# Kernel tuning notes

Hardware: AMD Instinct MI355X
Metric: run time of the kernel (lower is better)

## Reference

```python
import jax, jax.numpy as jnp
import numpy as np
import math

B, L, C, H, CP = 2, 512, 576, 8, 128
C3 = C // 3            # 192
DK = C // H            # 72
DK3 = DK // 3          # 24
DIV = math.sqrt(DK)


def _ln(x, w, b, eps=1e-6):
    m = jnp.mean(x, axis=-1, keepdims=True)
    v = jnp.mean(jnp.square(x - m), axis=-1, keepdims=True)
    return (x - m) * jax.lax.rsqrt(v + eps) * w + b


def setup_inputs() -> dict:
    key = jax.random.key(0)
    ks = jax.random.split(key, 12)
    s = 0.05
    def n(k, shape):
        return jax.random.normal(k, shape, jnp.float32) * s
    return {
        "x": jax.random.normal(ks[0], (B, L, C), jnp.float32),
        "pairX": jax.random.normal(ks[1], (B, L, L, CP), jnp.float32),
        "g": jnp.ones((1,), jnp.float32),
        "ln1_w": jnp.ones((C,), jnp.float32), "ln1_b": jnp.zeros((C,), jnp.float32),
        "ln2_w": jnp.ones((CP,), jnp.float32), "ln2_b": jnp.zeros((CP,), jnp.float32),
        "Wq": n(ks[2], (C3, C3)), "bq": jnp.zeros((C3,), jnp.float32),
        "Wk": n(ks[3], (C3, C3)), "bk": jnp.zeros((C3,), jnp.float32),
        "Wv": n(ks[4], (C3, C3)), "bv": jnp.zeros((C3,), jnp.float32),
        "Wg": n(ks[5], (C3, C3)), "bg": jnp.zeros((C3,), jnp.float32),
        "conv_w": n(ks[6], (3, H, H, 5, 5)), "conv_b": jnp.zeros((3, H), jnp.float32),
        "Wp": n(ks[7], (CP, H)), "bp": jnp.zeros((H,), jnp.float32),
        "Wpr": n(ks[8], (H, CP)), "bpr": jnp.zeros((CP,), jnp.float32),
        "Wo": n(ks[9], (C, C)), "bo": jnp.zeros((C,), jnp.float32),
    }


def reference(x, pairX, g, ln1_w, ln1_b, ln2_w, ln2_b, Wq, bq, Wk, bk, Wv, bv,
              Wg, bg, conv_w, conv_b, Wp, bp, Wpr, bpr, Wo, bo):
    ori_x = x
    xn = _ln(x, ln1_w, ln1_b)                      # [B,L,C]
    pn = _ln(pairX, ln2_w, ln2_b)                  # [B,L,L,CP]

    # split channels into 3 groups: [B,3,L,C3]
    xs = xn.reshape(B, L, 3, C3).transpose(0, 2, 1, 3)

    def proj(W, b):
        y = xs @ W + b                              # [B,3,L,C3]
        return y.reshape(B, 3, L, H, DK3).transpose(0, 1, 3, 2, 4)  # [B,3,H,L,DK3]

    q = proj(Wq, bq)
    k = proj(Wk, bk)
    v = proj(Wv, bv)
    gate = proj(Wg, bg)

    qkMatrix = jnp.einsum('bchld,bchmd->bchlm', q, k)  # [B,3,H,L,L]
    pairBias = (pn @ Wp + bp).transpose(0, 3, 1, 2)[:, None]  # [B,1,H,L,L]
    oriQK = qkMatrix + pairBias                     # [B,3,H,L,L]

    # 3-channel 5x5 conv refinement, summed over the 3 branches -> [B,1,H,L,L]
    dn = ('NCHW', 'OIHW', 'NCHW')
    convQK = sum(
        jax.lax.conv_general_dilated(oriQK[:, i], conv_w[i], (1, 1), 'SAME',
                                     dimension_numbers=dn)
        + conv_b[i][None, :, None, None]
        for i in range(3)
    )[:, None]

    qk = (oriQK + convQK) / DIV                     # [B,3,H,L,L]
    score = jax.nn.softmax(qk, axis=-1)
    h_outs = jnp.einsum('bchlm,bchmd->bchld', score, v) * jax.nn.sigmoid(gate)
    h_outs = h_outs.transpose(0, 3, 1, 2, 4).reshape(B, L, C)

    rawScoreMean = jax.nn.gelu(jnp.mean(qk, axis=1).transpose(0, 2, 3, 1),
                               approximate=False)   # [B,L,L,H]
    out1 = (h_outs @ Wo + bo) + ori_x * g
    out2 = rawScoreMean @ Wpr + bpr                 # [B,L,L,CP]
    return out1, out2
```

## Files before the change

kernel.cpp:

```cpp
#include <hip/hip_runtime.h>
#include <hip/hip_bf16.h>

#define BDIM 2
#define LDIM 512
#define CDIM 576
#define HDIM 8
#define CPD  128
#define DK3  24
#define INV_DIV 0.117851130197757920f

static constexpr size_t OFF_Q    = 0;
static constexpr size_t OFF_K    = 589824;
static constexpr size_t OFF_V    = 1179648;
static constexpr size_t OFF_G    = 1769472;
static constexpr size_t OFF_BIAS = 2359296;
static constexpr size_t OFF_ORI  = OFF_BIAS + 4194304;
static constexpr size_t OFF_QK   = OFF_ORI + 12582912;
static constexpr size_t OFF_H    = OFF_QK + 12582912;
static constexpr size_t OFF_WPH  = OFF_H + 589824;
static constexpr size_t OFF_CS   = OFF_WPH + 1024;
static constexpr size_t OFF_XN   = OFF_QK;

__device__ __forceinline__ float gelu_exact(float v) {
    return 0.5f * v * (1.f + erff(v * 0.70710678118654752f));
}

__global__ __launch_bounds__(256) void k_prep(
    const float* __restrict__ ln2w, const float* __restrict__ ln2b,
    const float* __restrict__ Wp, const float* __restrict__ bp,
    float* __restrict__ wph, float* __restrict__ csum)
{
    __shared__ float wl[1024];
    const int tid = threadIdx.x;
    for (int i = tid; i < 1024; i += 256) {
        int h = i >> 7, d = i & 127;
        float v = ln2w[d] * Wp[d * 8 + h];
        wl[i] = v; wph[i] = v;
    }
    __syncthreads();
    const int h = tid >> 5, c4 = tid & 31;
    float p = wl[h * 128 + c4 * 4] + wl[h * 128 + c4 * 4 + 1]
            + wl[h * 128 + c4 * 4 + 2] + wl[h * 128 + c4 * 4 + 3];
#pragma unroll
    for (int o = 1; o < 32; o <<= 1) p += __shfl_xor(p, o);
    if (c4 == 0) csum[h] = p;
    float q = 0.f;
#pragma unroll
    for (int k = 0; k < 4; ++k) { int d = c4 * 4 + k; q = fmaf(ln2b[d], Wp[d * 8 + h], q); }
#pragma unroll
    for (int o = 1; o < 32; o <<= 1) q += __shfl_xor(q, o);
    if (c4 == 0) csum[8 + h] = q + bp[h];
}

__global__ __launch_bounds__(256) void k_ln(
    const float* __restrict__ x, const float* __restrict__ ln1w, const float* __restrict__ ln1b,
    float* __restrict__ xn)
{
    const int tid = threadIdx.x;
    const int wid = tid >> 6, lane = tid & 63;
    const int row = blockIdx.x * 4 + wid;
    const float* xr = x + (size_t)row * CDIM;
    float vals[9]; float s = 0.f, sq = 0.f;
#pragma unroll
    for (int u = 0; u < 9; ++u) {
        float v = xr[lane + 64 * u];
        vals[u] = v; s += v; sq += v * v;
    }
#pragma unroll
    for (int o = 32; o; o >>= 1) { s += __shfl_xor(s, o); sq += __shfl_xor(sq, o); }
    float m = s * (1.f / 576.f);
    float inv = rsqrtf(sq * (1.f / 576.f) - m * m + 1e-6f);
    float* xo = xn + (size_t)row * CDIM;
#pragma unroll
    for (int u = 0; u < 9; ++u) {
        int idx = lane + 64 * u;
        xo[idx] = (vals[u] - m) * inv * ln1w[idx] + ln1b[idx];
    }
}

__global__ __launch_bounds__(256) void k_proj(
    const float* __restrict__ xn,
    const float* __restrict__ Wq, const float* __restrict__ bq,
    const float* __restrict__ Wk, const float* __restrict__ bk,
    const float* __restrict__ Wv, const float* __restrict__ bv,
    const float* __restrict__ Wg, const float* __restrict__ bg,
    float* __restrict__ qo, float* __restrict__ ko, float* __restrict__ vo, float* __restrict__ go)
{
    __shared__ float As[192 * 64];
    __shared__ float Bs[32 * 192];
    const int tid = threadIdx.x;
    const int bx = blockIdx.x;
    const int mi = bx / 48, rem = bx % 48;
    const int g = rem >> 4, rb = rem & 15;
    const int row0 = rb * 64;

    const float* W  = mi == 0 ? Wq : mi == 1 ? Wk : mi == 2 ? Wv : Wg;
    const float* bb = mi == 0 ? bq : mi == 1 ? bk : mi == 2 ? bv : bg;
    float* op       = mi == 0 ? qo : mi == 1 ? ko : mi == 2 ? vo : go;

    {
        const int r = tid & 63, k4b = tid >> 6;
#pragma unroll
        for (int it = 0; it < 12; ++it) {
            int k4 = k4b + it * 4;
            float4 v = *(const float4*)&xn[(size_t)(row0 + r) * 576 + g * 192 + k4 * 4];
            As[(k4 * 4 + 0) * 64 + r] = v.x;
            As[(k4 * 4 + 1) * 64 + r] = v.y;
            As[(k4 * 4 + 2) * 64 + r] = v.z;
            As[(k4 * 4 + 3) * 64 + r] = v.w;
        }
    }

    const int rg = tid >> 4, cg = tid & 15;
    const int r0 = rg * 4, c0 = cg * 12;
    float acc[4][12] = {};

    for (int kk = 0; kk < 192; kk += 32) {
        __syncthreads();
#pragma unroll
        for (int i = 0; i < 6; ++i) {
            int f = tid + 256 * i;
            int k2 = f / 48, c4 = f % 48;
            *(float4*)&Bs[k2 * 192 + c4 * 4] = *(const float4*)&W[(size_t)(kk + k2) * 192 + c4 * 4];
        }
        __syncthreads();
#pragma unroll
        for (int k2 = 0; k2 < 32; ++k2) {
            const float4 a  = *(const float4*)&As[(kk + k2) * 64 + r0];
            const float4 b0 = *(const float4*)&Bs[k2 * 192 + c0];
            const float4 b1 = *(const float4*)&Bs[k2 * 192 + c0 + 4];
            const float4 b2 = *(const float4*)&Bs[k2 * 192 + c0 + 8];
            const float ar[4] = {a.x, a.y, a.z, a.w};
#pragma unroll
            for (int r = 0; r < 4; ++r) {
                acc[r][0] = fmaf(ar[r], b0.x, acc[r][0]);
                acc[r][1] = fmaf(ar[r], b0.y, acc[r][1]);
                acc[r][2] = fmaf(ar[r], b0.z, acc[r][2]);
                acc[r][3] = fmaf(ar[r], b0.w, acc[r][3]);
                acc[r][4] = fmaf(ar[r], b1.x, acc[r][4]);
                acc[r][5] = fmaf(ar[r], b1.y, acc[r][5]);
                acc[r][6] = fmaf(ar[r], b1.z, acc[r][6]);
                acc[r][7] = fmaf(ar[r], b1.w, acc[r][7]);
                acc[r][8] = fmaf(ar[r], b2.x, acc[r][8]);
                acc[r][9] = fmaf(ar[r], b2.y, acc[r][9]);
                acc[r][10] = fmaf(ar[r], b2.z, acc[r][10]);
                acc[r][11] = fmaf(ar[r], b2.w, acc[r][11]);
            }
        }
    }

    const int h = cg >> 1, d24 = (cg & 1) * 12;
    const float4 bj0 = *(const float4*)&bb[c0];
    const float4 bj1 = *(const float4*)&bb[c0 + 4];
    const float4 bj2 = *(const float4*)&bb[c0 + 8];
#pragma unroll
    for (int r = 0; r < 4; ++r) {
        int row = row0 + r0 + r;
        int b = row >> 9, l = row & 511;
        float* o = op + ((((size_t)b * 3 + g) * HDIM + h) * LDIM + l) * DK3 + d24;
        *(float4*)(o + 0) = make_float4(acc[r][0] + bj0.x, acc[r][1] + bj0.y,
                                        acc[r][2] + bj0.z, acc[r][3] + bj0.w);
        *(float4*)(o + 4) = make_float4(acc[r][4] + bj1.x, acc[r][5] + bj1.y,
                                        acc[r][6] + bj1.z, acc[r][7] + bj1.w);
        *(float4*)(o + 8) = make_float4(acc[r][8] + bj2.x, acc[r][9] + bj2.y,
                                        acc[r][10] + bj2.z, acc[r][11] + bj2.w);
    }
}

__global__ __launch_bounds__(256) void k_pairbias(
    const float* __restrict__ pairX, const float* __restrict__ wph,
    const float* __restrict__ csum, float* __restrict__ bias)
{
    const int row = blockIdx.x * 256 + threadIdx.x;
    const float* rp = pairX + (size_t)row * CPD;

    float acc[8] = {};
    float sum = 0.f, sumsq = 0.f;
    for (int s = 0; s < 8; ++s) {
        float rr[16];
        *(float4*)&rr[0]  = *(const float4*)(rp + s * 16 + 0);
        *(float4*)&rr[4]  = *(const float4*)(rp + s * 16 + 4);
        *(float4*)&rr[8]  = *(const float4*)(rp + s * 16 + 8);
        *(float4*)&rr[12] = *(const float4*)(rp + s * 16 + 12);
#pragma unroll
        for (int k = 0; k < 16; ++k) { sum += rr[k]; sumsq = fmaf(rr[k], rr[k], sumsq); }
        const float* wp_s = wph + s * 16;
#pragma unroll
        for (int h = 0; h < 8; ++h) {
            const float* w = wp_s + h * 128;
#pragma unroll
            for (int k = 0; k < 16; ++k) acc[h] = fmaf(rr[k], w[k], acc[h]);
        }
    }
    const float m = sum * (1.f / 128.f);
    const float inv = rsqrtf(sumsq * (1.f / 128.f) - m * m + 1e-6f);
    const int b = row >> 18;
    const int ij = row & 262143;
    float* bo = bias + ((size_t)b << 21) + ij;
#pragma unroll
    for (int h = 0; h < 8; ++h) {
        float o = inv * (acc[h] - m * csum[h]) + csum[8 + h];
        bo[(size_t)h << 18] = o;
    }
}

__global__ __launch_bounds__(256) void k_qkmat(
    const float* __restrict__ q, const float* __restrict__ k,
    const float* __restrict__ bias, float* __restrict__ oriQK)
{
    __shared__ float Kl[512 * 28];
    __shared__ float Ql[32 * 28];
    const int tid = threadIdx.x;
    const int bch = blockIdx.x >> 4;
    const int itile = blockIdx.x & 15;
    const float* kp = k + (size_t)bch * 512 * 24;
    const float* qp = q + (size_t)bch * 512 * 24 + (size_t)itile * 32 * 24;
    for (int idx = tid; idx < 512 * 24; idx += 256) {
        int j = idx / 24, d = idx - j * 24;
        Kl[j * 28 + d] = kp[idx];
    }
    for (int idx = tid; idx < 32 * 24; idx += 256) {
        int i = idx / 24, d = idx - i * 24;
        Ql[i * 28 + d] = qp[idx];
    }
    __syncthreads();

    const int ti = tid >> 4, tj = tid & 15;
    const int b = bch / 24, h = bch & 7;
    const float* biasp = bias + ((size_t)(b * 8 + h) * 512 + itile * 32) * 512;
    float* outp = oriQK + (size_t)bch * 262144 + (size_t)itile * 32 * 512;

    for (int cc = 0; cc < 4; ++cc) {
        float acc[2][8] = {};
#pragma unroll
        for (int d4 = 0; d4 < 6; ++d4) {
            const float4 q0 = *(const float4*)&Ql[(ti * 2 + 0) * 28 + d4 * 4];
            const float4 q1 = *(const float4*)&Ql[(ti * 2 + 1) * 28 + d4 * 4];
#pragma unroll
            for (int u = 0; u < 8; ++u) {
                const float4 kv = *(const float4*)&Kl[(cc * 128 + u * 16 + tj) * 28 + d4 * 4];
                acc[0][u] = fmaf(q0.x, kv.x, fmaf(q0.y, kv.y, fmaf(q0.z, kv.z, fmaf(q0.w, kv.w, acc[0][u]))));
                acc[1][u] = fmaf(q1.x, kv.x, fmaf(q1.y, kv.y, fmaf(q1.z, kv.z, fmaf(q1.w, kv.w, acc[1][u]))));
            }
        }
#pragma unroll
        for (int r = 0; r < 2; ++r) {
            int i = ti * 2 + r;
#pragma unroll
            for (int u = 0; u < 8; ++u) {
                int j = cc * 128 + u * 16 + tj;
                outp[(size_t)i * 512 + j] = acc[r][u] + biasp[(size_t)i * 512 + j];
            }
        }
    }
}

__global__ __launch_bounds__(256, 2) void k_conv(
    const float* __restrict__ oriQK, const float* __restrict__ convW, const float* __restrict__ convB,
    const float* __restrict__ Wpr, const float* __restrict__ bpr,
    float* __restrict__ qk, float* __restrict__ out2)
{
    __shared__ float tile[8 * 36 * 40];
    __shared__ float gql[8 * 1024];
    const int tid = threadIdx.x;
    const int bx = blockIdx.x;
    const int b = bx >> 8, rem = bx & 255;
    const int i0 = (rem >> 4) * 32, j0 = (rem & 15) * 32;

    const int jg = tid & 7, ii = tid >> 3;
    const int j4 = jg * 4;
    float acc[8][4] = {};
    float cen[3][8][4];

    for (int c = 0; c < 3; ++c) {
        __syncthreads();
        for (int idx = tid; idx < 8 * 1296; idx += 256) {
            int ch = idx / 1296;
            int r = idx - ch * 1296;
            int iw = r / 36, jw = r - iw * 36;
            int gi = i0 - 2 + iw, gj = j0 - 2 + jw;
            float v = 0.f;
            if ((unsigned)gi < 512u && (unsigned)gj < 512u)
                v = oriQK[((size_t)(b * 24 + c * 8 + ch) << 18) + ((size_t)gi << 9) + gj];
            tile[ch * 1440 + iw * 40 + jw] = v;
        }
        __syncthreads();

        const float* wb = convW + c * 1600;
        for (int hi = 0; hi < 8; ++hi) {
            const float* tch = &tile[hi * 1440];
#pragma unroll
            for (int kh = 0; kh < 5; ++kh) {
                const float* trow = &tch[(ii + kh) * 40 + j4];
                float v[8];
                *(float4*)&v[0] = *(const float4*)&trow[0];
                *(float4*)&v[4] = *(const float4*)&trow[4];
#pragma unroll
                for (int kw = 0; kw < 5; ++kw) {
                    const float* wt = wb + hi * 25 + kh * 5 + kw;
                    const float w0 = wt[0],    w1 = wt[200],  w2 = wt[400],  w3 = wt[600];
                    const float w4 = wt[800],  w5 = wt[1000], w6 = wt[1200], w7 = wt[1400];
#pragma unroll
                    for (int j = 0; j < 4; ++j) {
                        float vv = v[kw + j];
                        acc[0][j] = fmaf(w0, vv, acc[0][j]);
                        acc[1][j] = fmaf(w1, vv, acc[1][j]);
                        acc[2][j] = fmaf(w2, vv, acc[2][j]);
                        acc[3][j] = fmaf(w3, vv, acc[3][j]);
                        acc[4][j] = fmaf(w4, vv, acc[4][j]);
                        acc[5][j] = fmaf(w5, vv, acc[5][j]);
                        acc[6][j] = fmaf(w6, vv, acc[6][j]);
                        acc[7][j] = fmaf(w7, vv, acc[7][j]);
                    }
                }
            }
        }
#pragma unroll
        for (int h = 0; h < 8; ++h) {
            const float* tr = &tile[h * 1440 + (ii + 2) * 40 + j4 + 2];
            cen[c][h][0] = tr[0]; cen[c][h][1] = tr[1];
            cen[c][h][2] = tr[2]; cen[c][h][3] = tr[3];
        }
    }

    const int gi = i0 + ii, gj = j0 + j4;
    float* qkb = qk + ((size_t)(b * 24) << 18) + ((size_t)gi << 9) + gj;
#pragma unroll
    for (int h = 0; h < 8; ++h) {
        float cv = convB[h] + convB[8 + h] + convB[16 + h];
        float cj[4];
#pragma unroll
        for (int j = 0; j < 4; ++j) cj[j] = acc[h][j] + cv;
        float mm[4] = {};
#pragma unroll
        for (int c = 0; c < 3; ++c) {
            float4 o = make_float4((cen[c][h][0] + cj[0]) * INV_DIV,
                                   (cen[c][h][1] + cj[1]) * INV_DIV,
                                   (cen[c][h][2] + cj[2]) * INV_DIV,
                                   (cen[c][h][3] + cj[3]) * INV_DIV);
            *(float4*)(qkb + ((size_t)(c * 8 + h) << 18)) = o;
#pragma unroll
            for (int j = 0; j < 4; ++j) mm[j] += cen[c][h][j];
        }
#pragma unroll
        for (int j = 0; j < 4; ++j) {
            float gv = gelu_exact((mm[j] * (1.f / 3.f) + cj[j]) * INV_DIV);
            gql[h * 1024 + ii * 32 + j4 + j] = gv;
        }
    }
    __syncthreads();

    const int pq = tid & 31, pg = tid >> 5;
    float4 wv[8];
#pragma unroll
    for (int h = 0; h < 8; ++h) wv[h] = *(const float4*)&Wpr[h * 128 + pq * 4];
    const float4 bv = *(const float4*)&bpr[pq * 4];

    for (int it = 0; it < 128; ++it) {
        int pos = it * 8 + pg;
        float g8[8];
#pragma unroll
        for (int h = 0; h < 8; ++h) g8[h] = gql[h * 1024 + pos];
        float4 o = bv;
        o.x += g8[0]*wv[0].x + g8[1]*wv[1].x + g8[2]*wv[2].x + g8[3]*wv[3].x
             + g8[4]*wv[4].x + g8[5]*wv[5].x + g8[6]*wv[6].x + g8[7]*wv[7].x;
        o.y += g8[0]*wv[0].y + g8[1]*wv[1].y + g8[2]*wv[2].y + g8[3]*wv[3].y
             + g8[4]*wv[4].y + g8[5]*wv[5].y + g8[6]*wv[6].y + g8[7]*wv[7].y;
        o.z += g8[0]*wv[0].z + g8[1]*wv[1].z + g8[2]*wv[2].z + g8[3]*wv[3].z
             + g8[4]*wv[4].z + g8[5]*wv[5].z + g8[6]*wv[6].z + g8[7]*wv[7].z;
        o.w += g8[0]*wv[0].w + g8[1]*wv[1].w + g8[2]*wv[2].w + g8[3]*wv[3].w
             + g8[4]*wv[4].w + g8[5]*wv[5].w + g8[6]*wv[6].w + g8[7]*wv[7].w;
        int oi = i0 + (pos >> 5), oj = j0 + (pos & 31);
        *(float4*)&out2[(((size_t)(b * 512 + oi) << 9) + oj) * 128 + pq * 4] = o;
    }
}

__global__ __launch_bounds__(256) void k_softmax_pv(
    const float* __restrict__ qk, const float* __restrict__ v, const float* __restrict__ gate,
    float* __restrict__ houts)
{
    __shared__ float Vl[512 * 28];
    const int tid = threadIdx.x;
    const int bch = blockIdx.x >> 4, itile = blockIdx.x & 15;
    const float* vp = v + (size_t)bch * (512 * 24);
    for (int idx = tid; idx < 512 * 24; idx += 256) {
        int j = idx / 24, d = idx - j * 24;
        Vl[j * 28 + d] = vp[idx];
    }
    __syncthreads();

    const int wid = tid >> 6, lane = tid & 63;
    const int b = bch / 24, c = (bch % 24) >> 3, h = bch & 7;
    const int tg = lane >> 3;
    for (int rr = 0; rr < 8; ++rr) {
        const int i = itile * 32 + wid * 8 + rr;
        const float* row = qk + ((size_t)bch * 512 + i) * 512;
        float e[8]; float mx = -1e30f;
#pragma unroll
        for (int u = 0; u < 8; ++u) { e[u] = row[lane + 64 * u]; mx = fmaxf(mx, e[u]); }
#pragma unroll
        for (int o = 32; o; o >>= 1) mx = fmaxf(mx, __shfl_xor(mx, o));
        float s = 0.f;
#pragma unroll
        for (int u = 0; u < 8; ++u) { e[u] = __expf(e[u] - mx); s += e[u]; }
#pragma unroll
        for (int o = 32; o; o >>= 1) s += __shfl_xor(s, o);
        float inv = 1.f / s;

        float4 a4[6] = {};
#pragma unroll
        for (int u = 0; u < 8; ++u) {
            float p = e[u] * inv;
            const float* vr = &Vl[(u * 64 + lane) * 28];
#pragma unroll
            for (int k = 0; k < 6; ++k) {
                float4 vv = *(const float4*)(vr + 4 * k);
                a4[k].x = fmaf(p, vv.x, a4[k].x);
                a4[k].y = fmaf(p, vv.y, a4[k].y);
                a4[k].z = fmaf(p, vv.z, a4[k].z);
                a4[k].w = fmaf(p, vv.w, a4[k].w);
            }
        }
#pragma unroll
        for (int k = 0; k < 6; ++k) {
            a4[k].x += __shfl_xor(a4[k].x, 8);  a4[k].y += __shfl_xor(a4[k].y, 8);
            a4[k].z += __shfl_xor(a4[k].z, 8);  a4[k].w += __shfl_xor(a4[k].w, 8);
            a4[k].x += __shfl_xor(a4[k].x, 16); a4[k].y += __shfl_xor(a4[k].y, 16);
            a4[k].z += __shfl_xor(a4[k].z, 16); a4[k].w += __shfl_xor(a4[k].w, 16);
            a4[k].x += __shfl_xor(a4[k].x, 32); a4[k].y += __shfl_xor(a4[k].y, 32);
            a4[k].z += __shfl_xor(a4[k].z, 32); a4[k].w += __shfl_xor(a4[k].w, 32);
        }
        const float af[24] = {
            a4[0].x, a4[0].y, a4[0].z, a4[0].w, a4[1].x, a4[1].y, a4[1].z, a4[1].w,
            a4[2].x, a4[2].y, a4[2].z, a4[2].w, a4[3].x, a4[3].y, a4[3].z, a4[3].w,
            a4[4].x, a4[4].y, a4[4].z, a4[4].w, a4[5].x, a4[5].y, a4[5].z, a4[5].w };
        float w0 = tg==0?af[0]:tg==1?af[3]:tg==2?af[6]:tg==3?af[9]:tg==4?af[12]:tg==5?af[15]:tg==6?af[18]:af[21];
        float w1 = tg==0?af[1]:tg==1?af[4]:tg==2?af[7]:tg==3?af[10]:tg==4?af[13]:tg==5?af[16]:tg==6?af[19]:af[22];
        float w2 = tg==0?af[2]:tg==1?af[5]:tg==2?af[8]:tg==3?af[11]:tg==4?af[14]:tg==5?af[17]:tg==6?af[20]:af[23];
#pragma unroll
        for (int o = 1; o < 8; o <<= 1) {
            w0 += __shfl_xor(w0, o);
            w1 += __shfl_xor(w1, o);
            w2 += __shfl_xor(w2, o);
        }
        if ((lane & 7) == 0) {
            const int d0 = tg * 3;
            const float* gp = gate + ((size_t)bch * 512 + i) * 24 + d0;
            float* op = houts + ((size_t)(b * 512 + i)) * 576 + c * 192 + h * 24 + d0;
            op[0] = w0 / (1.f + __expf(-gp[0]));
            op[1] = w1 / (1.f + __expf(-gp[1]));
            op[2] = w2 / (1.f + __expf(-gp[2]));
        }
    }
}

__global__ __launch_bounds__(256) void k_out1(
    const float* __restrict__ houts, const float* __restrict__ Wo, const float* __restrict__ bo,
    const float* __restrict__ x, const float* __restrict__ gsc,
    float* __restrict__ out1)
{
    __shared__ float As[32 * 33];
    __shared__ float Bs[32 * 64];
    const int tid = threadIdx.x;
    const int mt = blockIdx.x / 9, nt = blockIdx.x % 9;
    const int m0 = mt * 32, n0 = nt * 64;
    const int tn = tid & 15, tm = tid >> 4;
    float acc[2][4] = {};

    for (int kk = 0; kk < 576; kk += 32) {
        {
            int idx = tid;
#pragma unroll
            for (int i = 0; i < 4; ++i, idx += 256) {
                int k2 = idx & 31, m = idx >> 5;
                As[m * 33 + k2] = houts[(size_t)(m0 + m) * 576 + kk + k2];
            }
        }
        {
            int idx = tid;
#pragma unroll
            for (int i = 0; i < 8; ++i, idx += 256) {
                int n = idx & 63, k2 = idx >> 6;
                Bs[k2 * 64 + n] = Wo[(size_t)(kk + k2) * 576 + n0 + n];
            }
        }
        __syncthreads();
#pragma unroll
        for (int k2 = 0; k2 < 32; ++k2) {
            float a0 = As[(tm * 2 + 0) * 33 + k2];
            float a1 = As[(tm * 2 + 1) * 33 + k2];
            const float4 bv = *(const float4*)&Bs[k2 * 64 + tn * 4];
            acc[0][0] += a0 * bv.x; acc[0][1] += a0 * bv.y; acc[0][2] += a0 * bv.z; acc[0][3] += a0 * bv.w;
            acc[1][0] += a1 * bv.x; acc[1][1] += a1 * bv.y; acc[1][2] += a1 * bv.z; acc[1][3] += a1 * bv.w;
        }
        __syncthreads();
    }

    const float gv = gsc[0];
    const float4 b4 = *(const float4*)&bo[n0 + tn * 4];
#pragma unroll
    for (int r = 0; r < 2; ++r) {
        size_t row = (size_t)m0 + tm * 2 + r;
        size_t off = row * 576 + n0 + tn * 4;
        const float4 x4 = *(const float4*)&x[off];
        float4 o;
        o.x = acc[r][0] + b4.x + x4.x * gv;
        o.y = acc[r][1] + b4.y + x4.y * gv;
        o.z = acc[r][2] + b4.z + x4.z * gv;
        o.w = acc[r][3] + b4.w + x4.w * gv;
        *(float4*)&out1[off] = o;
    }
}

extern "C" void kernel_launch(void* const* d_in, const int* in_sizes, int n_in,
                              void* d_out, int out_size, void* d_ws, size_t ws_size,
                              hipStream_t stream) {
    const float* x     = (const float*)d_in[0];
    const float* pairX = (const float*)d_in[1];
    const float* g     = (const float*)d_in[2];
    const float* ln1w  = (const float*)d_in[3];
    const float* ln1b  = (const float*)d_in[4];
    const float* ln2w  = (const float*)d_in[5];
    const float* ln2b  = (const float*)d_in[6];
    const float* Wq    = (const float*)d_in[7];
    const float* bq    = (const float*)d_in[8];
    const float* Wk    = (const float*)d_in[9];
    const float* bk    = (const float*)d_in[10];
    const float* Wv    = (const float*)d_in[11];
    const float* bv    = (const float*)d_in[12];
    const float* Wg    = (const float*)d_in[13];
    const float* bg    = (const float*)d_in[14];
    const float* convW = (const float*)d_in[15];
    const float* convB = (const float*)d_in[16];
    const float* Wp    = (const float*)d_in[17];
    const float* bp    = (const float*)d_in[18];
    const float* Wpr   = (const float*)d_in[19];
    const float* bpr   = (const float*)d_in[20];
    const float* Wo    = (const float*)d_in[21];
    const float* bo    = (const float*)d_in[22];

    float* ws   = (float*)d_ws;
    float* q    = ws + OFF_Q;
    float* k    = ws + OFF_K;
    float* vv   = ws + OFF_V;
    float* gt   = ws + OFF_G;
    float* bias = ws + OFF_BIAS;
    float* ori  = ws + OFF_ORI;
    float* qkb  = ws + OFF_QK;
    float* xn   = ws + OFF_XN;
    float* hout = ws + OFF_H;
    float* wph  = ws + OFF_WPH;
    float* csum = ws + OFF_CS;

    float* out1 = (float*)d_out;
    float* out2 = out1 + 589824;

    k_prep<<<dim3(1), dim3(256), 0, stream>>>(ln2w, ln2b, Wp, bp, wph, csum);
    k_ln<<<dim3(256), dim3(256), 0, stream>>>(x, ln1w, ln1b, xn);
    k_proj<<<dim3(192), dim3(256), 0, stream>>>(xn, Wq, bq, Wk, bk, Wv, bv, Wg, bg,
                                                q, k, vv, gt);
    k_pairbias<<<dim3(2048), dim3(256), 0, stream>>>(pairX, wph, csum, bias);
    k_qkmat<<<dim3(768), dim3(256), 0, stream>>>(q, k, bias, ori);
    k_conv<<<dim3(512), dim3(256), 0, stream>>>(ori, convW, convB, Wpr, bpr, qkb, out2);
    k_softmax_pv<<<dim3(768), dim3(256), 0, stream>>>(qkb, vv, gt, hout);
    k_out1<<<dim3(288), dim3(256), 0, stream>>>(hout, Wo, bo, x, g, out1);
}
```

Measured before the change: 460.8 us.

## Split conv input-channel reduction across two thread halves in k_conv

Doubles k_conv's block size to 512 threads. Each half of the block convolves half of the input heads, and the partial sums are reduced through shared memory. The epilogue then runs on the first half only, and all 512 threads share the Wpr projection loop. This raises parallelism within each of the 512 blocks to hide latency, at the cost of an extra shared-memory reduction, more synchronisation, and idle threads during the epilogue.

Result: no change. 470.0 us (+2.0%).

```diff
diff --git a/kernel.cpp b/kernel.cpp
--- a/kernel.cpp
+++ b/kernel.cpp
@@ -255,26 +255,27 @@
     }
 }
 
-__global__ __launch_bounds__(256, 2) void k_conv(
+__global__ __launch_bounds__(512, 4) void k_conv(
     const float* __restrict__ oriQK, const float* __restrict__ convW, const float* __restrict__ convB,
     const float* __restrict__ Wpr, const float* __restrict__ bpr,
     float* __restrict__ qk, float* __restrict__ out2)
 {
     __shared__ float tile[8 * 36 * 40];
-    __shared__ float gql[8 * 1024];
+    __shared__ float scratch[8192];
     const int tid = threadIdx.x;
     const int bx = blockIdx.x;
     const int b = bx >> 8, rem = bx & 255;
     const int i0 = (rem >> 4) * 32, j0 = (rem & 15) * 32;
 
-    const int jg = tid & 7, ii = tid >> 3;
+    const int jg = tid & 7, ii = (tid >> 3) & 31;
+    const int rep = tid >> 8;
     const int j4 = jg * 4;
     float acc[8][4] = {};
     float cen[3][8][4];
 
     for (int c = 0; c < 3; ++c) {
         __syncthreads();
-        for (int idx = tid; idx < 8 * 1296; idx += 256) {
+        for (int idx = tid; idx < 8 * 1296; idx += 512) {
             int ch = idx / 1296;
             int r = idx - ch * 1296;
             int iw = r / 36, jw = r - iw * 36;
@@ -287,7 +288,7 @@
         __syncthreads();
 
         const float* wb = convW + c * 1600;
-        for (int hi = 0; hi < 8; ++hi) {
+        for (int hi = rep; hi < 8; hi += 2) {
             const float* tch = &tile[hi * 1440];
 #pragma unroll
             for (int kh = 0; kh < 5; ++kh) {
@@ -315,37 +316,61 @@
                 }
             }
         }
+        if (rep == 0) {
+#pragma unroll
+            for (int h = 0; h < 8; ++h) {
+                const float* tr = &tile[h * 1440 + (ii + 2) * 40 + j4 + 2];
+                cen[c][h][0] = tr[0]; cen[c][h][1] = tr[1];
+                cen[c][h][2] = tr[2]; cen[c][h][3] = tr[3];
+            }
+        }
+    }
+
+    if (rep == 1) {
+        const int s = tid - 256;
+#pragma unroll
+        for (int h = 0; h < 8; ++h)
+#pragma unroll
+            for (int j = 0; j < 4; ++j)
+                scratch[(h * 4 + j) * 256 + s] = acc[h][j];
+    }
+    __syncthreads();
+    if (rep == 0) {
+#pragma unroll
+        for (int h = 0; h < 8; ++h)
+#pragma unroll
+            for (int j = 0; j < 4; ++j)
+                acc[h][j] += scratch[(h * 4 + j) * 256 + tid];
+    }
+    __syncthreads();
+
+    float* gql = scratch;
+    if (rep == 0) {
+        const int gi = i0 + ii, gj = j0 + j4;
+        float* qkb = qk + ((size_t)(b * 24) << 18) + ((size_t)gi << 9) + gj;
 #pragma unroll
         for (int h = 0; h < 8; ++h) {
-            const float* tr = &tile[h * 1440 + (ii + 2) * 40 + j4 + 2];
-            cen[c][h][0] = tr[0]; cen[c][h][1] = tr[1];
-            cen[c][h][2] = tr[2]; cen[c][h][3] = tr[3];
-        }
-    }
-
-    const int gi = i0 + ii, gj = j0 + j4;
-    float* qkb = qk + ((size_t)(b * 24) << 18) + ((size_t)gi << 9) + gj;
-#pragma unroll
-    for (int h = 0; h < 8; ++h) {
-        float cv = convB[h] + convB[8 + h] + convB[16 + h];
-        float cj[4];
-#pragma unroll
-        for (int j = 0; j < 4; ++j) cj[j] = acc[h][j] + cv;
-        float mm[4] = {};
-#pragma unroll
-        for (int c = 0; c < 3; ++c) {
-            float4 o = make_float4((cen[c][h][0] + cj[0]) * INV_DIV,
-                                   (cen[c][h][1] + cj[1]) * INV_DIV,
-                                   (cen[c][h][2] + cj[2]) * INV_DIV,
-                                   (cen[c][h][3] + cj[3]) * INV_DIV);
-            *(float4*)(qkb + ((size_t)(c * 8 + h) << 18)) = o;
-#pragma unroll
-            for (int j = 0; j < 4; ++j) mm[j] += cen[c][h][j];
-        }
-#pragma unroll
-        for (int j = 0; j < 4; ++j) {
-            float gv = gelu_exact((mm[j] * (1.f / 3.f) + cj[j]) * INV_DIV);
-            gql[h * 1024 + ii * 32 + j4 + j] = gv;
+            float cv = convB[h] + convB[8 + h] + convB[16 + h];
+            float cj[4];
+#pragma unroll
+            for (int j = 0; j < 4; ++j) cj[j] = acc[h][j] + cv;
+            float mm[4] = {};
+#pragma unroll
+            for (int c = 0; c < 3; ++c) {
+                float4 o = make_float4((cen[c][h][0] + cj[0]) * INV_DIV,
+                                       (cen[c][h][1] + cj[1]) * INV_DIV,
+                                       (cen[c][h][2] + cj[2]) * INV_DIV,
+                                       (cen[c][h][3] + cj[3]) * INV_DIV);
+                *(float4*)(qkb + ((size_t)(c * 8 + h) << 18)) = o;
+#pragma unroll
+                for (int j = 0; j < 4; ++j) mm[j] += cen[c][h][j];
+            }
+            float4 gv4;
+            gv4.x = gelu_exact((mm[0] * (1.f / 3.f) + cj[0]) * INV_DIV);
+            gv4.y = gelu_exact((mm[1] * (1.f / 3.f) + cj[1]) * INV_DIV);
+            gv4.z = gelu_exact((mm[2] * (1.f / 3.f) + cj[2]) * INV_DIV);
+            gv4.w = gelu_exact((mm[3] * (1.f / 3.f) + cj[3]) * INV_DIV);
+            *(float4*)&gql[h * 1024 + ii * 32 + j4] = gv4;
         }
     }
     __syncthreads();
@@ -356,8 +381,8 @@
     for (int h = 0; h < 8; ++h) wv[h] = *(const float4*)&Wpr[h * 128 + pq * 4];
     const float4 bv = *(const float4*)&bpr[pq * 4];
 
-    for (int it = 0; it < 128; ++it) {
-        int pos = it * 8 + pg;
+    for (int it = 0; it < 64; ++it) {
+        int pos = it * 16 + pg;
         float g8[8];
 #pragma unroll
         for (int h = 0; h < 8; ++h) g8[h] = gql[h * 1024 + pos];
@@ -561,7 +586,7 @@
                                                 q, k, vv, gt);
     k_pairbias<<<dim3(2048), dim3(256), 0, stream>>>(pairX, wph, csum, bias);
     k_qkmat<<<dim3(768), dim3(256), 0, stream>>>(q, k, bias, ori);
-    k_conv<<<dim3(512), dim3(256), 0, stream>>>(ori, convW, convB, Wpr, bpr, qkb, out2);
+    k_conv<<<dim3(512), dim3(512), 0, stream>>>(ori, convW, convB, Wpr, bpr, qkb, out2);
     k_softmax_pv<<<dim3(768), dim3(256), 0, stream>>>(qkb, vv, gt, hout);
     k_out1<<<dim3(288), dim3(256), 0, stream>>>(hout, Wo, bo, x, g, out1);
 }
```

## Cut k_conv registers and LDS, stage transposed conv weights, use nontemporal stores

Applied to the files above, without the earlier changes.

The conv kernel now copies the conv weights into shared memory in an [hi][tap][h] layout, so each tap's eight output-channel weights come in as two float4 LDS reads instead of eight scalar global loads. The per-c center values are no longer kept in registers; they are re-read from global oriQK in the epilogue. The gelu staging buffer reuses the tile array, which frees LDS and, with launch bounds raised to 3 blocks per CU, is meant to increase occupancy. The out1/out2 writes become nontemporal stores, at the cost of extra global reads of oriQK and possible register spills under the tighter bound.

Measured after the change: 430.8 us. 6.5% less time.

```diff
diff --git a/kernel.cpp b/kernel.cpp
--- a/kernel.cpp
+++ b/kernel.cpp
@@ -23,6 +23,12 @@
 
 __device__ __forceinline__ float gelu_exact(float v) {
     return 0.5f * v * (1.f + erff(v * 0.70710678118654752f));
+}
+
+typedef float __attribute__((ext_vector_type(4))) f32x4;
+__device__ __forceinline__ void nt_store4(float* p, float a, float b, float c, float d) {
+    f32x4 t = {a, b, c, d};
+    __builtin_nontemporal_store(t, (f32x4*)p);
 }
 
 __global__ __launch_bounds__(256) void k_prep(
@@ -255,13 +261,13 @@
     }
 }
 
-__global__ __launch_bounds__(256, 2) void k_conv(
+__global__ __launch_bounds__(256, 3) void k_conv(
     const float* __restrict__ oriQK, const float* __restrict__ convW, const float* __restrict__ convB,
     const float* __restrict__ Wpr, const float* __restrict__ bpr,
     float* __restrict__ qk, float* __restrict__ out2)
 {
     __shared__ float tile[8 * 36 * 40];
-    __shared__ float gql[8 * 1024];
+    __shared__ float wT[1600];
     const int tid = threadIdx.x;
     const int bx = blockIdx.x;
     const int b = bx >> 8, rem = bx & 255;
@@ -270,10 +276,14 @@
     const int jg = tid & 7, ii = tid >> 3;
     const int j4 = jg * 4;
     float acc[8][4] = {};
-    float cen[3][8][4];
 
     for (int c = 0; c < 3; ++c) {
         __syncthreads();
+        for (int i = tid; i < 1600; i += 256) {
+            int h = i & 7, rest = i >> 3;
+            int tap = rest % 25, hi = rest / 25;
+            wT[hi * 200 + tap * 8 + h] = convW[c * 1600 + h * 200 + hi * 25 + tap];
+        }
         for (int idx = tid; idx < 8 * 1296; idx += 256) {
             int ch = idx / 1296;
             int r = idx - ch * 1296;
@@ -286,9 +296,9 @@
         }
         __syncthreads();
 
-        const float* wb = convW + c * 1600;
         for (int hi = 0; hi < 8; ++hi) {
             const float* tch = &tile[hi * 1440];
+            const float* wch = &wT[hi * 200];
 #pragma unroll
             for (int kh = 0; kh < 5; ++kh) {
                 const float* trow = &tch[(ii + kh) * 40 + j4];
@@ -297,57 +307,66 @@
                 *(float4*)&v[4] = *(const float4*)&trow[4];
 #pragma unroll
                 for (int kw = 0; kw < 5; ++kw) {
-                    const float* wt = wb + hi * 25 + kh * 5 + kw;
-                    const float w0 = wt[0],    w1 = wt[200],  w2 = wt[400],  w3 = wt[600];
-                    const float w4 = wt[800],  w5 = wt[1000], w6 = wt[1200], w7 = wt[1400];
+                    const float4 wA = *(const float4*)&wch[(kh * 5 + kw) * 8];
+                    const float4 wB = *(const float4*)&wch[(kh * 5 + kw) * 8 + 4];
 #pragma unroll
                     for (int j = 0; j < 4; ++j) {
                         float vv = v[kw + j];
-                        acc[0][j] = fmaf(w0, vv, acc[0][j]);
-                        acc[1][j] = fmaf(w1, vv, acc[1][j]);
-                        acc[2][j] = fmaf(w2, vv, acc[2][j]);
-                        acc[3][j] = fmaf(w3, vv, acc[3][j]);
-                        acc[4][j] = fmaf(w4, vv, acc[4][j]);
-                        acc[5][j] = fmaf(w5, vv, acc[5][j]);
-                        acc[6][j] = fmaf(w6, vv, acc[6][j]);
-                        acc[7][j] = fmaf(w7, vv, acc[7][j]);
+                        acc[0][j] = fmaf(wA.x, vv, acc[0][j]);
+                        acc[1][j] = fmaf(wA.y, vv, acc[1][j]);
+                        acc[2][j] = fmaf(wA.z, vv, acc[2][j]);
+                        acc[3][j] = fmaf(wA.w, vv, acc[3][j]);
+                        acc[4][j] = fmaf(wB.x, vv, acc[4][j]);
+                        acc[5][j] = fmaf(wB.y, vv, acc[5][j]);
+                        acc[6][j] = fmaf(wB.z, vv, acc[6][j]);
+                        acc[7][j] = fmaf(wB.w, vv, acc[7][j]);
                     }
                 }
             }
         }
-#pragma unroll
-        for (int h = 0; h < 8; ++h) {
-            const float* tr = &tile[h * 1440 + (ii + 2) * 40 + j4 + 2];
-            cen[c][h][0] = tr[0]; cen[c][h][1] = tr[1];
-            cen[c][h][2] = tr[2]; cen[c][h][3] = tr[3];
-        }
     }
 
     const int gi = i0 + ii, gj = j0 + j4;
+    const float* orib = oriQK + ((size_t)(b * 24) << 18) + ((size_t)gi << 9) + gj;
     float* qkb = qk + ((size_t)(b * 24) << 18) + ((size_t)gi << 9) + gj;
-#pragma unroll
-    for (int h = 0; h < 8; ++h) {
-        float cv = convB[h] + convB[8 + h] + convB[16 + h];
-        float cj[4];
-#pragma unroll
-        for (int j = 0; j < 4; ++j) cj[j] = acc[h][j] + cv;
-        float mm[4] = {};
-#pragma unroll
-        for (int c = 0; c < 3; ++c) {
-            float4 o = make_float4((cen[c][h][0] + cj[0]) * INV_DIV,
-                                   (cen[c][h][1] + cj[1]) * INV_DIV,
-                                   (cen[c][h][2] + cj[2]) * INV_DIV,
-                                   (cen[c][h][3] + cj[3]) * INV_DIV);
-            *(float4*)(qkb + ((size_t)(c * 8 + h) << 18)) = o;
-#pragma unroll
-            for (int j = 0; j < 4; ++j) mm[j] += cen[c][h][j];
-        }
-#pragma unroll
-        for (int j = 0; j < 4; ++j) {
-            float gv = gelu_exact((mm[j] * (1.f / 3.f) + cj[j]) * INV_DIV);
-            gql[h * 1024 + ii * 32 + j4 + j] = gv;
-        }
-    }
+    float4 gv4[2];
+#pragma unroll
+    for (int hq = 0; hq < 2; ++hq) {
+        float gvt[4];
+#pragma unroll
+        for (int hh = 0; hh < 4; ++hh) {
+            const int h = hq * 4 + hh;
+            float cv = convB[h] + convB[8 + h] + convB[16 + h];
+            float cj[4];
+#pragma unroll
+            for (int j = 0; j < 4; ++j) cj[j] = acc[h][j] + cv;
+            float mm[4] = {};
+#pragma unroll
+            for (int c = 0; c < 3; ++c) {
+                const float4 t = *(const float4*)(orib + ((size_t)(c * 8 + h) << 18));
+                mm[0] += t.x; mm[1] += t.y; mm[2] += t.z; mm[3] += t.w;
+                float4 o = make_float4((t.x + cj[0]) * INV_DIV, (t.y + cj[1]) * INV_DIV,
+                                       (t.z + cj[2]) * INV_DIV, (t.w + cj[3]) * INV_DIV);
+                *(float4*)(qkb + ((size_t)(c * 8 + h) << 18)) = o;
+            }
+            gvt[hh] = 0.f;
+            mm[0] = gelu_exact((mm[0] * (1.f / 3.f) + cj[0]) * INV_DIV);
+            mm[1] = gelu_exact((mm[1] * (1.f / 3.f) + cj[1]) * INV_DIV);
+            mm[2] = gelu_exact((mm[2] * (1.f / 3.f) + cj[2]) * INV_DIV);
+            mm[3] = gelu_exact((mm[3] * (1.f / 3.f) + cj[3]) * INV_DIV);
+            if (hq == 0) {
+                if (hh == 0) gv4[0] = make_float4(mm[0], mm[1], mm[2], mm[3]);
+            }
+            acc[h][0] = mm[0]; acc[h][1] = mm[1]; acc[h][2] = mm[2]; acc[h][3] = mm[3];
+        }
+        (void)gvt;
+    }
+    __syncthreads();
+
+    float* gql = tile;
+#pragma unroll
+    for (int h = 0; h < 8; ++h)
+        *(float4*)&gql[h * 1024 + ii * 32 + j4] = make_float4(acc[h][0], acc[h][1], acc[h][2], acc[h][3]);
     __syncthreads();
 
     const int pq = tid & 31, pg = tid >> 5;
@@ -361,17 +380,16 @@
         float g8[8];
 #pragma unroll
         for (int h = 0; h < 8; ++h) g8[h] = gql[h * 1024 + pos];
-        float4 o = bv;
-        o.x += g8[0]*wv[0].x + g8[1]*wv[1].x + g8[2]*wv[2].x + g8[3]*wv[3].x
-             + g8[4]*wv[4].x + g8[5]*wv[5].x + g8[6]*wv[6].x + g8[7]*wv[7].x;
-        o.y += g8[0]*wv[0].y + g8[1]*wv[1].y + g8[2]*wv[2].y + g8[3]*wv[3].y
-             + g8[4]*wv[4].y + g8[5]*wv[5].y + g8[6]*wv[6].y + g8[7]*wv[7].y;
-        o.z += g8[0]*wv[0].z + g8[1]*wv[1].z + g8[2]*wv[2].z + g8[3]*wv[3].z
-             + g8[4]*wv[4].z + g8[5]*wv[5].z + g8[6]*wv[6].z + g8[7]*wv[7].z;
-        o.w += g8[0]*wv[0].w + g8[1]*wv[1].w + g8[2]*wv[2].w + g8[3]*wv[3].w
-             + g8[4]*wv[4].w + g8[5]*wv[5].w + g8[6]*wv[6].w + g8[7]*wv[7].w;
+        float ox = bv.x + g8[0]*wv[0].x + g8[1]*wv[1].x + g8[2]*wv[2].x + g8[3]*wv[3].x
+                 + g8[4]*wv[4].x + g8[5]*wv[5].x + g8[6]*wv[6].x + g8[7]*wv[7].x;
+        float oy = bv.y + g8[0]*wv[0].y + g8[1]*wv[1].y + g8[2]*wv[2].y + g8[3]*wv[3].y
+                 + g8[4]*wv[4].y + g8[5]*wv[5].y + g8[6]*wv[6].y + g8[7]*wv[7].y;
+        float oz = bv.z + g8[0]*wv[0].z + g8[1]*wv[1].z + g8[2]*wv[2].z + g8[3]*wv[3].z
+                 + g8[4]*wv[4].z + g8[5]*wv[5].z + g8[6]*wv[6].z + g8[7]*wv[7].z;
+        float ow = bv.w + g8[0]*wv[0].w + g8[1]*wv[1].w + g8[2]*wv[2].w + g8[3]*wv[3].w
+                 + g8[4]*wv[4].w + g8[5]*wv[5].w + g8[6]*wv[6].w + g8[7]*wv[7].w;
         int oi = i0 + (pos >> 5), oj = j0 + (pos & 31);
-        *(float4*)&out2[(((size_t)(b * 512 + oi) << 9) + oj) * 128 + pq * 4] = o;
+        nt_store4(&out2[(((size_t)(b * 512 + oi) << 9) + oj) * 128 + pq * 4], ox, oy, oz, ow);
     }
 }
 
@@ -503,12 +521,11 @@
         size_t row = (size_t)m0 + tm * 2 + r;
         size_t off = row * 576 + n0 + tn * 4;
         const float4 x4 = *(const float4*)&x[off];
-        float4 o;
-        o.x = acc[r][0] + b4.x + x4.x * gv;
-        o.y = acc[r][1] + b4.y + x4.y * gv;
-        o.z = acc[r][2] + b4.z + x4.z * gv;
-        o.w = acc[r][3] + b4.w + x4.w * gv;
-        *(float4*)&out1[off] = o;
+        nt_store4(&out1[off],
+                  acc[r][0] + b4.x + x4.x * gv,
+                  acc[r][1] + b4.y + x4.y * gv,
+                  acc[r][2] + b4.z + x4.z * gv,
+                  acc[r][3] + b4.w + x4.w * gv);
     }
 }
 
```
